# Kernel optimization log

Hardware: AMD Instinct MI355X
Metric: run time of the kernel (lower is better)

Reference implementation:

```python
import jax, jax.numpy as jnp
import numpy as np

B, C, CI, H, W = 4, 128, 64, 64, 64


def conv1x1(x, w, b):
    # x: [B,C,H,W], w: [Cout,Cin], b: [Cout]
    return jnp.einsum('bchw,oc->bohw', x, w) + b[None, :, None, None]


def setup_inputs() -> dict:
    key = jax.random.key(0)
    ks = jax.random.split(key, 10)
    s = 0.05  # keep logits in a sane range for softmax
    return {
        'x0': jax.random.normal(ks[0], (B, C, H, W), jnp.float32),
        'x1': jax.random.normal(ks[1], (B, C, H, W), jnp.float32),
        'g_w': jax.random.normal(ks[2], (CI, C), jnp.float32) * s,
        'g_b': jax.random.normal(ks[3], (CI,), jnp.float32) * s,
        'theta_w': jax.random.normal(ks[4], (CI, C), jnp.float32) * s,
        'theta_b': jax.random.normal(ks[5], (CI,), jnp.float32) * s,
        'phi_w': jax.random.normal(ks[6], (CI, C), jnp.float32) * s,
        'phi_b': jax.random.normal(ks[7], (CI,), jnp.float32) * s,
        'W_w': jax.random.normal(ks[8], (C, CI), jnp.float32) * s,
        'W_b': jax.random.normal(ks[9], (C,), jnp.float32) * s,
    }


def reference(x0, x1, g_w, g_b, theta_w, theta_b, phi_w, phi_b, W_w, W_b):
    b, c, h, w = x0.shape
    n = h * w
    ci = g_w.shape[0]
    g_x = conv1x1(x0, g_w, g_b).reshape(b, ci, n).transpose(0, 2, 1)      # [B,N,Ci]
    theta_x = conv1x1(x1, theta_w, theta_b).reshape(b, ci, n).transpose(0, 2, 1)  # [B,N,Ci]
    phi_x = conv1x1(x0, phi_w, phi_b).reshape(b, ci, n)                    # [B,Ci,N]
    f = jnp.einsum('bqc,bck->bqk', theta_x, phi_x)                         # [B,N,N]
    f_div_C = jax.nn.softmax(f, axis=-1)
    y = jnp.einsum('bqk,bkc->bqc', f_div_C, g_x)                           # [B,N,Ci]
    y = y.transpose(0, 2, 1).reshape(b, ci, h, w)
    W_y = conv1x1(y, W_w, W_b)
    return W_y + x0
```

## Files before the change

### kernel.cpp

```cpp
#include <hip/hip_runtime.h>
#include <hip/hip_bf16.h>


typedef unsigned int   u32;
typedef unsigned short u16;
typedef __attribute__((ext_vector_type(8))) short short8;
typedef __attribute__((ext_vector_type(4))) short short4v;
typedef __attribute__((ext_vector_type(4))) float f32x4;

#define LOG2E 1.4426950408889634f
#define KSPLIT 8

__device__ __forceinline__ float b2f(u16 v) {
  union { u32 u; float f; } x; x.u = ((u32)v) << 16; return x.f;
}
__device__ __forceinline__ u16 f2b(float f) {
  u32 u = __float_as_uint(f);
  return (u16)((u + 0x8000u) >> 16);
}
__device__ __forceinline__ short8 load_w_frag(const float* p, float s) {
  const float4 f0 = ((const float4*)p)[0];
  const float4 f1 = ((const float4*)p)[1];
  union { u32 w[4]; short8 s8; } r;
  r.w[0] = (u32)f2b(f0.x * s) | ((u32)f2b(f0.y * s) << 16);
  r.w[1] = (u32)f2b(f0.z * s) | ((u32)f2b(f0.w * s) << 16);
  r.w[2] = (u32)f2b(f1.x * s) | ((u32)f2b(f1.y * s) << 16);
  r.w[3] = (u32)f2b(f1.z * s) | ((u32)f2b(f1.w * s) << 16);
  return r.s8;
}


__global__ __launch_bounds__(256) void qkv_fused_kernel(
    const float* __restrict__ x0, const float* __restrict__ x1,
    const float* __restrict__ tw, const float* __restrict__ tb,
    const float* __restrict__ pw, const float* __restrict__ pb,
    const float* __restrict__ gw, const float* __restrict__ gb,
    u16* __restrict__ Q, u16* __restrict__ K, u16* __restrict__ Vt)
{
  const int n0 = blockIdx.x * 64;
  const int b  = blockIdx.y;
  const int t  = threadIdx.x;

  __shared__ __align__(16) short xt[2][64][136];

  #pragma unroll
  for (int i = 0; i < 16; ++i) {
    const int idx = i * 256 + t;
    const int tensor = idx >> 11;
    const int c  = (idx >> 4) & 127;
    const int n4 = idx & 15;
    const float4 v = *(const float4*)(
        (tensor ? x1 : x0) + ((size_t)b * 128 + c) * 4096 + n0 + n4 * 4);
    short* d = &xt[tensor][n4 * 4][c];
    d[0]       = (short)f2b(v.x);
    d[136]     = (short)f2b(v.y);
    d[2 * 136] = (short)f2b(v.z);
    d[3 * 136] = (short)f2b(v.w);
  }
  asm volatile("" ::: "memory");
  __syncthreads();

  const int wave = t >> 6;
  const int lane = t & 63;
  const int quad = lane >> 4, l15 = lane & 15;

  if (wave < 2) {
    const int conv = wave;
    const float* wsrc = conv ? pw : tw;
    const float  ws   = conv ? 1.f : LOG2E;
    const short* xl   = &xt[conv ? 0 : 1][0][0];

    f32x4 acc[4][4];
    #pragma unroll
    for (int i = 0; i < 4; ++i)
      #pragma unroll
      for (int j = 0; j < 4; ++j) acc[i][j] = (f32x4){0.f, 0.f, 0.f, 0.f};

    #pragma unroll
    for (int kk = 0; kk < 4; ++kk) {
      short8 wf[4], xf[4];
      #pragma unroll
      for (int ot = 0; ot < 4; ++ot)
        wf[ot] = load_w_frag(wsrc + (ot * 16 + l15) * 128 + kk * 32 + quad * 8, ws);
      #pragma unroll
      for (int nt = 0; nt < 4; ++nt)
        xf[nt] = *(const short8*)(xl + (nt * 16 + l15) * 136 + kk * 32 + quad * 8);
      #pragma unroll
      for (int i = 0; i < 4; ++i)
        #pragma unroll
        for (int j = 0; j < 4; ++j)
          acc[i][j] = __builtin_amdgcn_mfma_f32_16x16x32_bf16(xf[i], wf[j], acc[i][j], 0, 0, 0);
    }

    u16* dst = (conv ? K : Q) + (size_t)b * 4096 * 64;
    const float* bias = conv ? pb : tb;
    const float bscale = conv ? 1.f : LOG2E;
    #pragma unroll
    for (int ot = 0; ot < 4; ++ot) {
      const float bv = bias[ot * 16 + l15] * bscale;
      #pragma unroll
      for (int nt = 0; nt < 4; ++nt)
        #pragma unroll
        for (int r = 0; r < 4; ++r) {
          const int n = n0 + nt * 16 + quad * 4 + r;
          dst[(size_t)n * 64 + ot * 16 + l15] = f2b(acc[nt][ot][r] + bv);
        }
    }
  } else {
    const int oh = wave - 2;
    const short* xl = &xt[0][0][0];

    f32x4 acc[2][4];
    #pragma unroll
    for (int i = 0; i < 2; ++i)
      #pragma unroll
      for (int j = 0; j < 4; ++j) acc[i][j] = (f32x4){0.f, 0.f, 0.f, 0.f};

    #pragma unroll
    for (int kk = 0; kk < 4; ++kk) {
      short8 wf[2], xf[4];
      #pragma unroll
      for (int ot = 0; ot < 2; ++ot)
        wf[ot] = load_w_frag(gw + ((oh * 2 + ot) * 16 + l15) * 128 + kk * 32 + quad * 8, 1.f);
      #pragma unroll
      for (int nt = 0; nt < 4; ++nt)
        xf[nt] = *(const short8*)(xl + (nt * 16 + l15) * 136 + kk * 32 + quad * 8);
      #pragma unroll
      for (int i = 0; i < 2; ++i)
        #pragma unroll
        for (int j = 0; j < 4; ++j)
          acc[i][j] = __builtin_amdgcn_mfma_f32_16x16x32_bf16(wf[i], xf[j], acc[i][j], 0, 0, 0);
    }

    u16* dst = Vt + (size_t)b * 64 * 4096;
    #pragma unroll
    for (int ot = 0; ot < 2; ++ot)
      #pragma unroll
      for (int r = 0; r < 4; ++r) {
        const int o = (oh * 2 + ot) * 16 + quad * 4 + r;
        const float bv = gb[o];
        #pragma unroll
        for (int nc = 0; nc < 4; ++nc)
          dst[(size_t)o * 4096 + n0 + nc * 16 + l15] = f2b(acc[ot][nc][r] + bv);
      }
  }
}

__global__ __launch_bounds__(256, 4) void attn_kernel(
    const u16* __restrict__ Q, const u16* __restrict__ K,
    const u16* __restrict__ Vt, u16* __restrict__ Opart,
    float* __restrict__ Lp)
{
  const int qt = blockIdx.x, b = blockIdx.y, ks = blockIdx.z;
  const int tid  = threadIdx.x;
  const int wave = tid >> 6;
  const int lane = tid & 63;
  const int quad = lane >> 4;
  const int l15  = lane & 15;

  __shared__ __align__(16) short K_lds[2][64][72];
  __shared__ __align__(16) short V_lds[2][64][72];

  const int q0 = qt * 128 + wave * 32;
  const u16* Qb = Q  + (size_t)b * 4096 * 64;
  const u16* Kb = K  + (size_t)b * 4096 * 64;
  const u16* Vb = Vt + (size_t)b * 64 * 4096;

  const int kbase = ks * (4096 / KSPLIT);
  const int NKT   = 4096 / KSPLIT / 64;

  const int sr = tid >> 2;
  const int sc = (tid & 3) * 8;

  short8 qf[2][2];
  #pragma unroll
  for (int nt = 0; nt < 2; ++nt) {
    const u16* qp = Qb + (size_t)(q0 + nt * 16 + l15) * 64 + quad * 8;
    qf[nt][0] = *(const short8*)qp;
    qf[nt][1] = *(const short8*)(qp + 32);
  }

  f32x4 oacc[2][4];
  #pragma unroll
  for (int i = 0; i < 2; ++i)
    #pragma unroll
    for (int j = 0; j < 4; ++j)
      oacc[i][j] = (f32x4){0.f, 0.f, 0.f, 0.f};
  float lsum[2] = {0.f, 0.f};

  {
    const u16* kg = Kb + (size_t)kbase * 64;
    uint4 ra = *(const uint4*)(kg + (size_t)sr * 64 + sc);
    uint4 rb = *(const uint4*)(kg + (size_t)sr * 64 + sc + 32);
    uint4 rc = *(const uint4*)(Vb + (size_t)sr * 4096 + kbase + sc);
    uint4 rd = *(const uint4*)(Vb + (size_t)sr * 4096 + kbase + sc + 32);
    *(uint4*)&K_lds[0][sr][sc]      = ra;
    *(uint4*)&K_lds[0][sr][sc + 32] = rb;
    *(uint4*)&V_lds[0][sr][sc]      = rc;
    *(uint4*)&V_lds[0][sr][sc + 32] = rd;
  }
  __syncthreads();

  for (int kt = 0; kt < NKT; ++kt) {
    const int buf = kt & 1;
    const bool pre = (kt + 1 < NKT);

    uint4 kra, krb, vra, vrb;
    if (pre) {
      const int k1 = kbase + (kt + 1) * 64;
      const u16* kg = Kb + (size_t)k1 * 64;
      kra = *(const uint4*)(kg + (size_t)sr * 64 + sc);
      krb = *(const uint4*)(kg + (size_t)sr * 64 + sc + 32);
      vra = *(const uint4*)(Vb + (size_t)sr * 4096 + k1 + sc);
      vrb = *(const uint4*)(Vb + (size_t)sr * 4096 + k1 + sc + 32);
    }

    #pragma unroll
    for (int kh = 0; kh < 2; ++kh) {
      short8 kf[2][2];
      #pragma unroll
      for (int m = 0; m < 2; ++m) {
        kf[m][0] = *(const short8*)&K_lds[buf][(kh * 2 + m) * 16 + l15][quad * 8];
        kf[m][1] = *(const short8*)&K_lds[buf][(kh * 2 + m) * 16 + l15][quad * 8 + 32];
      }
      short8 vf[4];
      #pragma unroll
      for (int nd = 0; nd < 4; ++nd) {
        union { short4v h[2]; short8 s8; } vv;
        vv.h[0] = *(const short4v*)&V_lds[buf][nd * 16 + l15][kh * 32 + quad * 4];
        vv.h[1] = *(const short4v*)&V_lds[buf][nd * 16 + l15][kh * 32 + 16 + quad * 4];
        vf[nd] = vv.s8;
      }

      union { u32 w[4]; short8 s8; } pa[2];
      #pragma unroll
      for (int m = 0; m < 2; ++m) {
        #pragma unroll
        for (int nt = 0; nt < 2; ++nt) {
          f32x4 s = {0.f, 0.f, 0.f, 0.f};
          s = __builtin_amdgcn_mfma_f32_16x16x32_bf16(kf[m][0], qf[nt][0], s, 0, 0, 0);
          s = __builtin_amdgcn_mfma_f32_16x16x32_bf16(kf[m][1], qf[nt][1], s, 0, 0, 0);
          float p0 = exp2f(s[0]), p1 = exp2f(s[1]), p2 = exp2f(s[2]), p3 = exp2f(s[3]);
          lsum[nt] += (p0 + p1) + (p2 + p3);
          u32 u0 = __float_as_uint(p0) + 0x8000u;
          u32 u1 = __float_as_uint(p1) + 0x8000u;
          u32 u2 = __float_as_uint(p2) + 0x8000u;
          u32 u3 = __float_as_uint(p3) + 0x8000u;
          pa[nt].w[m * 2]     = __builtin_amdgcn_perm(u1, u0, 0x07060302u);
          pa[nt].w[m * 2 + 1] = __builtin_amdgcn_perm(u3, u2, 0x07060302u);
        }
      }

      #pragma unroll
      for (int nt = 0; nt < 2; ++nt)
        #pragma unroll
        for (int nd = 0; nd < 4; ++nd)
          oacc[nt][nd] = __builtin_amdgcn_mfma_f32_16x16x32_bf16(pa[nt].s8, vf[nd], oacc[nt][nd], 0, 0, 0);
    }

    if (pre) {
      const int nb = buf ^ 1;
      *(uint4*)&K_lds[nb][sr][sc]      = kra;
      *(uint4*)&K_lds[nb][sr][sc + 32] = krb;
      *(uint4*)&V_lds[nb][sr][sc]      = vra;
      *(uint4*)&V_lds[nb][sr][sc + 32] = vrb;
    }
    __syncthreads();
  }

  #pragma unroll
  for (int nt = 0; nt < 2; ++nt) {
    float v = lsum[nt];
    v += __shfl_xor(v, 16, 64);
    v += __shfl_xor(v, 32, 64);
    lsum[nt] = v;
  }
  float* LpB = Lp + ((size_t)ks * 4 + b) * 4096;
  if (quad == 0) {
    #pragma unroll
    for (int nt = 0; nt < 2; ++nt)
      LpB[q0 + nt * 16 + l15] = lsum[nt];
  }

  u16* Ob = Opart + ((size_t)ks * 4 + b) * 4096 * 64;
  #pragma unroll
  for (int mq = 0; mq < 2; ++mq)
    #pragma unroll
    for (int nd = 0; nd < 4; ++nd)
      #pragma unroll
      for (int r = 0; r < 4; ++r) {
        int q = q0 + mq * 16 + quad * 4 + r;
        Ob[(size_t)q * 64 + nd * 16 + l15] = f2b(oacc[mq][nd][r]);
      }
}

__global__ __launch_bounds__(256) void out_fused_kernel(
    const u16* __restrict__ Opart, const float* __restrict__ Lp,
    const float* __restrict__ Wf, const float* __restrict__ Wbf,
    const float* __restrict__ x0, float* __restrict__ out)
{
  const int n0 = blockIdx.x * 64;
  const int b  = blockIdx.y;
  const int t  = threadIdx.x;

  __shared__ __align__(16) short Ys[64][72];

  {
    const int nl = t >> 2;
    const int q4 = t & 3;
    const int ng = n0 + nl;

    float l = 0.f;
    #pragma unroll
    for (int ks = 0; ks < KSPLIT; ++ks)
      l += Lp[((size_t)ks * 4 + b) * 4096 + ng];

    float a[16];
    #pragma unroll
    for (int j = 0; j < 16; ++j) a[j] = 0.f;
    #pragma unroll
    for (int ks = 0; ks < KSPLIT; ++ks) {
      const uint4* row = (const uint4*)(Opart + (((size_t)ks * 4 + b) * 4096 + ng) * 64 + q4 * 16);
      #pragma unroll
      for (int v = 0; v < 2; ++v) {
        uint4 r = row[v];
        u32 wds[4] = {r.x, r.y, r.z, r.w};
        #pragma unroll
        for (int j = 0; j < 4; ++j) {
          a[v * 8 + 2 * j]     += __uint_as_float(wds[j] << 16);
          a[v * 8 + 2 * j + 1] += __uint_as_float(wds[j] & 0xffff0000u);
        }
      }
    }
    const float rinv = 1.f / l;
    union { u32 w[8]; short8 s8[2]; } pk;
    #pragma unroll
    for (int j = 0; j < 8; ++j)
      pk.w[j] = (u32)f2b(a[2 * j] * rinv) | ((u32)f2b(a[2 * j + 1] * rinv) << 16);
    *(short8*)&Ys[nl][q4 * 16]     = pk.s8[0];
    *(short8*)&Ys[nl][q4 * 16 + 8] = pk.s8[1];
  }
  asm volatile("" ::: "memory");
  __syncthreads();

  const int wave = t >> 6;
  const int lane = t & 63;
  const int quad = lane >> 4, l15 = lane & 15;

  f32x4 acc[2][4];
  #pragma unroll
  for (int i = 0; i < 2; ++i)
    #pragma unroll
    for (int j = 0; j < 4; ++j) acc[i][j] = (f32x4){0.f, 0.f, 0.f, 0.f};

  #pragma unroll
  for (int kk = 0; kk < 2; ++kk) {
    short8 wf[2], yf[4];
    #pragma unroll
    for (int ot = 0; ot < 2; ++ot)
      wf[ot] = load_w_frag(Wf + ((wave * 2 + ot) * 16 + l15) * 64 + kk * 32 + quad * 8, 1.f);
    #pragma unroll
    for (int nt = 0; nt < 4; ++nt)
      yf[nt] = *(const short8*)&Ys[nt * 16 + l15][kk * 32 + quad * 8];
    #pragma unroll
    for (int i = 0; i < 2; ++i)
      #pragma unroll
      for (int j = 0; j < 4; ++j)
        acc[i][j] = __builtin_amdgcn_mfma_f32_16x16x32_bf16(wf[i], yf[j], acc[i][j], 0, 0, 0);
  }

  #pragma unroll
  for (int ot = 0; ot < 2; ++ot)
    #pragma unroll
    for (int r = 0; r < 4; ++r) {
      const int o = (wave * 2 + ot) * 16 + quad * 4 + r;
      const float bv = Wbf[o];
      #pragma unroll
      for (int nt = 0; nt < 4; ++nt) {
        const size_t idx = ((size_t)(b * 128 + o)) * 4096 + n0 + nt * 16 + l15;
        out[idx] = acc[ot][nt][r] + bv + x0[idx];
      }
    }
}

extern "C" void kernel_launch(void* const* d_in, const int* in_sizes, int n_in,
                              void* d_out, int out_size, void* d_ws, size_t ws_size,
                              hipStream_t stream) {
  const float* x0 = (const float*)d_in[0];
  const float* x1 = (const float*)d_in[1];
  const float* gw = (const float*)d_in[2];
  const float* gb = (const float*)d_in[3];
  const float* tw = (const float*)d_in[4];
  const float* tb = (const float*)d_in[5];
  const float* pw = (const float*)d_in[6];
  const float* pb = (const float*)d_in[7];
  const float* Ww = (const float*)d_in[8];
  const float* Wb = (const float*)d_in[9];
  float* out = (float*)d_out;

  char* ws = (char*)d_ws;
  u16*   Qw    = (u16*)(ws + 0);
  u16*   Kw    = (u16*)(ws + (2u << 20));
  u16*   Vtw   = (u16*)(ws + (4u << 20));
  u16*   Opart = (u16*)(ws + (6u << 20));
  float* Lp    = (float*)(ws + (22u << 20));

  qkv_fused_kernel<<<dim3(64, 4), dim3(256), 0, stream>>>(
      x0, x1, tw, tb, pw, pb, gw, gb, Qw, Kw, Vtw);

  attn_kernel<<<dim3(32, 4, KSPLIT), dim3(256), 0, stream>>>(Qw, Kw, Vtw, Opart, Lp);

  out_fused_kernel<<<dim3(64, 4), dim3(256), 0, stream>>>(
      Opart, Lp, Ww, Wb, x0, out);
}
```

Measured before the change: 128.7 us.

## Shrink attention query tile to 16 rows per wave and halve key split

Each wave now handles 16 query rows instead of 32, so a block covers 64 queries, and the key dimension is split 4 ways instead of 8. The total block count stays the same (64x4x4 vs 32x4x8), but each block walks twice as many key tiles with less register pressure per wave. The partial-output buffer and the combine work in the output kernel shrink, at the cost of loading each K/V tile into LDS for fewer queries, which lowers reuse per load. This assumes out_fused_kernel reads KSPLIT partials through the macro.

```diff
diff --git a/kernel.cpp b/kernel.cpp
--- a/kernel.cpp
+++ b/kernel.cpp
@@ -9,7 +9,7 @@
 typedef __attribute__((ext_vector_type(4))) float f32x4;
 
 #define LOG2E 1.4426950408889634f
-#define KSPLIT 8
+#define KSPLIT 4
 
 __device__ __forceinline__ float b2f(u16 v) {
   union { u32 u; float f; } x; x.u = ((u32)v) << 16; return x.f;
@@ -161,7 +161,7 @@
   __shared__ __align__(16) short K_lds[2][64][72];
   __shared__ __align__(16) short V_lds[2][64][72];
 
-  const int q0 = qt * 128 + wave * 32;
+  const int q0 = qt * 64 + wave * 16;
   const u16* Qb = Q  + (size_t)b * 4096 * 64;
   const u16* Kb = K  + (size_t)b * 4096 * 64;
   const u16* Vb = Vt + (size_t)b * 64 * 4096;
@@ -172,21 +172,18 @@
   const int sr = tid >> 2;
   const int sc = (tid & 3) * 8;
 
-  short8 qf[2][2];
-  #pragma unroll
-  for (int nt = 0; nt < 2; ++nt) {
-    const u16* qp = Qb + (size_t)(q0 + nt * 16 + l15) * 64 + quad * 8;
-    qf[nt][0] = *(const short8*)qp;
-    qf[nt][1] = *(const short8*)(qp + 32);
-  }
-
-  f32x4 oacc[2][4];
-  #pragma unroll
-  for (int i = 0; i < 2; ++i)
-    #pragma unroll
-    for (int j = 0; j < 4; ++j)
-      oacc[i][j] = (f32x4){0.f, 0.f, 0.f, 0.f};
-  float lsum[2] = {0.f, 0.f};
+  short8 qf0, qf1;
+  {
+    const u16* qp = Qb + (size_t)(q0 + l15) * 64 + quad * 8;
+    qf0 = *(const short8*)qp;
+    qf1 = *(const short8*)(qp + 32);
+  }
+
+  f32x4 oacc[4];
+  #pragma unroll
+  for (int j = 0; j < 4; ++j)
+    oacc[j] = (f32x4){0.f, 0.f, 0.f, 0.f};
+  float lsum = 0.f;
 
   {
     const u16* kg = Kb + (size_t)kbase * 64;
@@ -232,30 +229,25 @@
         vf[nd] = vv.s8;
       }
 
-      union { u32 w[4]; short8 s8; } pa[2];
+      union { u32 w[4]; short8 s8; } pa;
       #pragma unroll
       for (int m = 0; m < 2; ++m) {
-        #pragma unroll
-        for (int nt = 0; nt < 2; ++nt) {
-          f32x4 s = {0.f, 0.f, 0.f, 0.f};
-          s = __builtin_amdgcn_mfma_f32_16x16x32_bf16(kf[m][0], qf[nt][0], s, 0, 0, 0);
-          s = __builtin_amdgcn_mfma_f32_16x16x32_bf16(kf[m][1], qf[nt][1], s, 0, 0, 0);
-          float p0 = exp2f(s[0]), p1 = exp2f(s[1]), p2 = exp2f(s[2]), p3 = exp2f(s[3]);
-          lsum[nt] += (p0 + p1) + (p2 + p3);
-          u32 u0 = __float_as_uint(p0) + 0x8000u;
-          u32 u1 = __float_as_uint(p1) + 0x8000u;
-          u32 u2 = __float_as_uint(p2) + 0x8000u;
-          u32 u3 = __float_as_uint(p3) + 0x8000u;
-          pa[nt].w[m * 2]     = __builtin_amdgcn_perm(u1, u0, 0x07060302u);
-          pa[nt].w[m * 2 + 1] = __builtin_amdgcn_perm(u3, u2, 0x07060302u);
-        }
-      }
-
-      #pragma unroll
-      for (int nt = 0; nt < 2; ++nt)
-        #pragma unroll
-        for (int nd = 0; nd < 4; ++nd)
-          oacc[nt][nd] = __builtin_amdgcn_mfma_f32_16x16x32_bf16(pa[nt].s8, vf[nd], oacc[nt][nd], 0, 0, 0);
+        f32x4 s = {0.f, 0.f, 0.f, 0.f};
+        s = __builtin_amdgcn_mfma_f32_16x16x32_bf16(kf[m][0], qf0, s, 0, 0, 0);
+        s = __builtin_amdgcn_mfma_f32_16x16x32_bf16(kf[m][1], qf1, s, 0, 0, 0);
+        float p0 = exp2f(s[0]), p1 = exp2f(s[1]), p2 = exp2f(s[2]), p3 = exp2f(s[3]);
+        lsum += (p0 + p1) + (p2 + p3);
+        u32 u0 = __float_as_uint(p0) + 0x8000u;
+        u32 u1 = __float_as_uint(p1) + 0x8000u;
+        u32 u2 = __float_as_uint(p2) + 0x8000u;
+        u32 u3 = __float_as_uint(p3) + 0x8000u;
+        pa.w[m * 2]     = __builtin_amdgcn_perm(u1, u0, 0x07060302u);
+        pa.w[m * 2 + 1] = __builtin_amdgcn_perm(u3, u2, 0x07060302u);
+      }
+
+      #pragma unroll
+      for (int nd = 0; nd < 4; ++nd)
+        oacc[nd] = __builtin_amdgcn_mfma_f32_16x16x32_bf16(pa.s8, vf[nd], oacc[nd], 0, 0, 0);
     }
 
     if (pre) {
@@ -268,30 +260,24 @@
     __syncthreads();
   }
 
-  #pragma unroll
-  for (int nt = 0; nt < 2; ++nt) {
-    float v = lsum[nt];
+  {
+    float v = lsum;
     v += __shfl_xor(v, 16, 64);
     v += __shfl_xor(v, 32, 64);
-    lsum[nt] = v;
+    lsum = v;
   }
   float* LpB = Lp + ((size_t)ks * 4 + b) * 4096;
-  if (quad == 0) {
-    #pragma unroll
-    for (int nt = 0; nt < 2; ++nt)
-      LpB[q0 + nt * 16 + l15] = lsum[nt];
-  }
+  if (quad == 0)
+    LpB[q0 + l15] = lsum;
 
   u16* Ob = Opart + ((size_t)ks * 4 + b) * 4096 * 64;
   #pragma unroll
-  for (int mq = 0; mq < 2; ++mq)
-    #pragma unroll
-    for (int nd = 0; nd < 4; ++nd)
-      #pragma unroll
-      for (int r = 0; r < 4; ++r) {
-        int q = q0 + mq * 16 + quad * 4 + r;
-        Ob[(size_t)q * 64 + nd * 16 + l15] = f2b(oacc[mq][nd][r]);
-      }
+  for (int nd = 0; nd < 4; ++nd)
+    #pragma unroll
+    for (int r = 0; r < 4; ++r) {
+      int q = q0 + quad * 4 + r;
+      Ob[(size_t)q * 64 + nd * 16 + l15] = f2b(oacc[nd][r]);
+    }
 }
 
 __global__ __launch_bounds__(256) void out_fused_kernel(
@@ -408,7 +394,7 @@
   qkv_fused_kernel<<<dim3(64, 4), dim3(256), 0, stream>>>(
       x0, x1, tw, tb, pw, pb, gw, gb, Qw, Kw, Vtw);
 
-  attn_kernel<<<dim3(32, 4, KSPLIT), dim3(256), 0, stream>>>(Qw, Kw, Vtw, Opart, Lp);
+  attn_kernel<<<dim3(64, 4, KSPLIT), dim3(256), 0, stream>>>(Qw, Kw, Vtw, Opart, Lp);
 
   out_fused_kernel<<<dim3(64, 4), dim3(256), 0, stream>>>(
       Opart, Lp, Ww, Wb, x0, out);
```

Measured after the change: 140.7 us. 9.3% more time.
